# Kernel tuning notes

Hardware: AMD Instinct MI355X
Metric: run time of the kernel (lower is better)

The kernel has to match this reference:

```python
import jax, jax.numpy as jnp
import numpy as np

VOCAB, HID, EMB = 32000, 8, 32
SEQ, BATCH = 64, 64


def setup_inputs() -> dict:
    key = jax.random.key(0)
    ks = jax.random.split(key, 16)
    D = EMB + HID
    def lin(k, fan_in, fan_out):
        # mimic nn.Linear default init: U(-1/sqrt(fan_in), 1/sqrt(fan_in))
        lim = 1.0 / np.sqrt(fan_in)
        kw, kb = jax.random.split(k)
        W = jax.random.uniform(kw, (fan_in, fan_out), jnp.float32, -lim, lim)
        b = jax.random.uniform(kb, (fan_out,), jnp.float32, -lim, lim)
        return W, b
    x = jax.random.randint(ks[0], (SEQ, BATCH), 0, VOCAB)
    embeddings = jax.random.normal(ks[1], (VOCAB, EMB), jnp.float32)
    Wz1, bz1 = lin(ks[2], D, 1)
    Wr1, br1 = lin(ks[3], D, 1)
    Wh1, bh1 = lin(ks[4], D, HID)
    Wz2, bz2 = lin(ks[5], D, 1)
    Wr2, br2 = lin(ks[6], D, 1)
    Wh2, bh2 = lin(ks[7], D, HID)
    Wout, bout = lin(ks[8], 2 * HID, VOCAB)
    return dict(x=x, embeddings=embeddings,
                Wz1=Wz1, bz1=bz1, Wr1=Wr1, br1=br1, Wh1=Wh1, bh1=bh1,
                Wz2=Wz2, bz2=bz2, Wr2=Wr2, br2=br2, Wh2=Wh2, bh2=bh2,
                Wout=Wout, bout=bout)


def _gru_scan(enc, Wz, bz, Wr, br, Wh, bh):
    # enc: [T, B, E]; emits the PRE-update hidden state at each step, matching
    # the original (total_h[t] = h before the step-t update; last update unused).
    B = enc.shape[1]
    H = Wh.shape[1]
    h0 = jnp.zeros((B, H), enc.dtype)
    def step(h, e):
        cat = jnp.concatenate([h, e], axis=1)          # [B, H+E]
        z = jax.nn.sigmoid(cat @ Wz + bz)              # [B, 1] -> broadcast over H
        r = jax.nn.sigmoid(cat @ Wr + br)
        h_cand = jnp.tanh(jnp.concatenate([r * h, e], axis=1) @ Wh + bh)
        h_new = (1.0 - z) * h + z * h_cand
        return h_new, h
    _, hs = jax.lax.scan(step, h0, enc)
    return hs                                          # [T, B, H]


def reference(x, embeddings, Wz1, bz1, Wr1, br1, Wh1, bh1,
              Wz2, bz2, Wr2, br2, Wh2, bh2, Wout, bout):
    enc = embeddings[x]                                # [T, B, E]
    h1 = _gru_scan(enc, Wz1, bz1, Wr1, br1, Wh1, bh1)  # forward direction
    h2 = _gru_scan(enc[::-1], Wz2, bz2, Wr2, br2, Wh2, bh2)[::-1]  # backward
    total_h = jnp.concatenate([h1, h2], axis=2)        # [T, B, 2H]
    logits = total_h @ Wout + bout                     # [T, B, V]
    return jax.nn.log_softmax(logits, axis=2)
```

## Files before the change

kernel.cpp:

```cpp
#include <hip/hip_runtime.h>

#define T 64
#define B 64
#define V 32000
#define E 32
#define H 8
#define PSTR 12

typedef float f32x4 __attribute__((ext_vector_type(4)));

__device__ __forceinline__ float fast_rcp(float x) { return __builtin_amdgcn_rcpf(x); }
__device__ __forceinline__ float sigmoid_f(float x) { return fast_rcp(1.0f + __expf(-x)); }
__device__ __forceinline__ float tanh_f(float x) { return 1.0f - 2.0f * fast_rcp(__expf(2.0f * x) + 1.0f); }

__global__ void __launch_bounds__(64) precompute_kernel(
    const int* __restrict__ x, const float* __restrict__ emb,
    const float* __restrict__ Wz1, const float* __restrict__ bz1,
    const float* __restrict__ Wr1, const float* __restrict__ br1,
    const float* __restrict__ Wh1, const float* __restrict__ bh1,
    const float* __restrict__ Wz2, const float* __restrict__ bz2,
    const float* __restrict__ Wr2, const float* __restrict__ br2,
    const float* __restrict__ Wh2, const float* __restrict__ bh2,
    float* __restrict__ pre)
{
    const int i = blockIdx.x;
    const int dir = blockIdx.y;
    const int b = threadIdx.x;

    const float* Wz = dir ? Wz2 : Wz1;  const float* bz = dir ? bz2 : bz1;
    const float* Wr = dir ? Wr2 : Wr1;  const float* br = dir ? br2 : br1;
    const float* Wh = dir ? Wh2 : Wh1;  const float* bh = dir ? bh2 : bh1;

    const int pos = dir ? (T - 1 - i) : i;
    const int idx = x[pos * B + b];

    float e[E];
    const float4* e4p = reinterpret_cast<const float4*>(emb + (size_t)idx * E);
#pragma unroll
    for (int q = 0; q < E / 4; q++) {
        float4 t = e4p[q];
        e[q*4+0] = t.x; e[q*4+1] = t.y; e[q*4+2] = t.z; e[q*4+3] = t.w;
    }

    float az = bz[0], ar = br[0];
    float ah[H];
#pragma unroll
    for (int j = 0; j < H; j++) ah[j] = bh[j];

#pragma unroll
    for (int d = 0; d < E; d++) {
        const float ed = e[d];
        az += ed * Wz[H + d];
        ar += ed * Wr[H + d];
#pragma unroll
        for (int j = 0; j < H; j++) ah[j] += ed * Wh[(H + d) * H + j];
    }

    float* dst = pre + ((size_t)dir * T * B + i * B + b) * PSTR;
    float4 s0 = {az, ar, ah[0], ah[1]};
    float4 s1 = {ah[2], ah[3], ah[4], ah[5]};
    float4 s2 = {ah[6], ah[7], 0.0f, 0.0f};
    *reinterpret_cast<float4*>(dst + 0) = s0;
    *reinterpret_cast<float4*>(dst + 4) = s1;
    *reinterpret_cast<float4*>(dst + 8) = s2;
}

__global__ void __launch_bounds__(64) gru_scan_kernel(
    const float* __restrict__ Wz1, const float* __restrict__ Wr1, const float* __restrict__ Wh1,
    const float* __restrict__ Wz2, const float* __restrict__ Wr2, const float* __restrict__ Wh2,
    const float* __restrict__ pre, float* __restrict__ th)
{
    const int dir = blockIdx.x;
    const int b = threadIdx.x;
    const float* Wz = dir ? Wz2 : Wz1;
    const float* Wr = dir ? Wr2 : Wr1;
    const float* Wh = dir ? Wh2 : Wh1;

    float wzh[H], wrh[H], whh[H * H];
#pragma unroll
    for (int k = 0; k < H; k++) { wzh[k] = Wz[k]; wrh[k] = Wr[k]; }
#pragma unroll
    for (int d = 0; d < H; d++)
#pragma unroll
        for (int j = 0; j < H; j++) whh[d * H + j] = Wh[d * H + j];

    float h[H];
#pragma unroll
    for (int j = 0; j < H; j++) h[j] = 0.0f;

    const float* preD = pre + (size_t)dir * T * B * PSTR;
    const float4* p4 = reinterpret_cast<const float4*>(preD + (size_t)b * PSTR);
    float4 p0 = p4[0], p1 = p4[1], p2 = p4[2];

    for (int i = 0; i < T; i++) {
        const int pos = dir ? (T - 1 - i) : i;

        float* dst = th + ((size_t)pos * B + b) * 16 + dir * 8;
        float4 s0 = {h[0], h[1], h[2], h[3]};
        float4 s1 = {h[4], h[5], h[6], h[7]};
        *reinterpret_cast<float4*>(dst + 0) = s0;
        *reinterpret_cast<float4*>(dst + 4) = s1;

        const float az = p0.x, ar = p0.y;
        float ah[H] = {p0.z, p0.w, p1.x, p1.y, p1.z, p1.w, p2.x, p2.y};

        const int ni = (i < T - 1) ? (i + 1) : (T - 1);
        const float4* n4 = reinterpret_cast<const float4*>(preD + ((size_t)ni * B + b) * PSTR);
        p0 = n4[0]; p1 = n4[1]; p2 = n4[2];

        float zx = az, rx = ar;
#pragma unroll
        for (int k = 0; k < H; k++) { zx += h[k] * wzh[k]; rx += h[k] * wrh[k]; }
        const float z = sigmoid_f(zx);
        const float r = sigmoid_f(rx);

        float hc[H];
#pragma unroll
        for (int j = 0; j < H; j++) hc[j] = ah[j];
#pragma unroll
        for (int d = 0; d < H; d++) {
            const float rh = r * h[d];
#pragma unroll
            for (int j = 0; j < H; j++) hc[j] += rh * whh[d * H + j];
        }
#pragma unroll
        for (int j = 0; j < H; j++) {
            const float c = tanh_f(hc[j]);
            h[j] += z * (c - h[j]);
        }
    }
}

#define R 16
#define RS 8
#define NG (R / RS)
#define V4 (V / 4)
#define K3_THREADS 512
#define K3_WAVES (K3_THREADS / 64)

__device__ __forceinline__ float4 dot16(const float4 bb, const float4* w, const float* hrow) {
    float ax = bb.x, ay = bb.y, az = bb.z, aw = bb.w;
#pragma unroll
    for (int k4 = 0; k4 < 4; k4++) {
        const float4 hh = *reinterpret_cast<const float4*>(hrow + k4 * 4);
        ax += hh.x * w[k4*4+0].x; ay += hh.x * w[k4*4+0].y; az += hh.x * w[k4*4+0].z; aw += hh.x * w[k4*4+0].w;
        ax += hh.y * w[k4*4+1].x; ay += hh.y * w[k4*4+1].y; az += hh.y * w[k4*4+1].z; aw += hh.y * w[k4*4+1].w;
        ax += hh.z * w[k4*4+2].x; ay += hh.z * w[k4*4+2].y; az += hh.z * w[k4*4+2].z; aw += hh.z * w[k4*4+2].w;
        ax += hh.w * w[k4*4+3].x; ay += hh.w * w[k4*4+3].y; az += hh.w * w[k4*4+3].z; aw += hh.w * w[k4*4+3].w;
    }
    return {ax, ay, az, aw};
}

template<int SE0, int SEN, int ST0, int STN>
__device__ __forceinline__ void k3_phase(
    const float4* __restrict__ W4, const float4* __restrict__ b4p,
    float* __restrict__ out, const float (&hlds)[R][16],
    float (&l)[R], const float (&lse)[R], int tid, int row0)
{
    for (int v4 = tid; v4 < V4; v4 += K3_THREADS) {
        asm volatile("" ::: "memory");
        float4 w[16];
#pragma unroll
        for (int k = 0; k < 16; k++) w[k] = W4[(size_t)k * V4 + v4];
        const float4 bb = b4p[v4];

#pragma unroll
        for (int r = 0; r < STN; r++) {
            const int rr = ST0 + r;
            const float4 o = dot16(bb, w, &hlds[rr][0]);
            f32x4 res = {o.x - lse[rr], o.y - lse[rr], o.z - lse[rr], o.w - lse[rr]};
            f32x4* dst = reinterpret_cast<f32x4*>(out + ((size_t)(row0 + rr) * V4 + v4) * 4);
            __builtin_nontemporal_store(res, dst);
        }
#pragma unroll
        for (int r = 0; r < SEN; r++) {
            const int rr = SE0 + r;
            const float4 o = dot16(bb, w, &hlds[rr][0]);
            l[rr] += (__expf(o.x) + __expf(o.y)) + (__expf(o.z) + __expf(o.w));
        }
    }
}

template<int G0>
__device__ __forceinline__ void k3_reduce(
    float (&l)[R], float (&lse)[R],
    float (*red)[K3_WAVES][RS], int tid)
{
    float v[RS];
#pragma unroll
    for (int r = 0; r < RS; r++) {
        v[r] = l[G0 + r];
#pragma unroll
        for (int m = 1; m < 64; m <<= 1) v[r] += __shfl_xor(v[r], m, 64);
    }
    const int lane = tid & 63, wid = tid >> 6;
    if (lane == 0) {
#pragma unroll
        for (int r = 0; r < RS; r++) red[G0 / RS][wid][r] = v[r];
    }
    __syncthreads();
#pragma unroll
    for (int r = 0; r < RS; r++) {
        float t = 0.0f;
#pragma unroll
        for (int w = 0; w < K3_WAVES; w++) t += red[G0 / RS][w][r];
        lse[G0 + r] = logf(t);
    }
}

__global__ void __launch_bounds__(K3_THREADS) logits_kernel(
    const float* __restrict__ th, const float* __restrict__ Wout,
    const float* __restrict__ bout, float* __restrict__ out)
{
    __shared__ __align__(16) float hlds[R][16];
    __shared__ float red[NG][K3_WAVES][RS];

    const int tid = threadIdx.x;
    const int row0 = blockIdx.x * R;

    if (tid < R * 4) {
        reinterpret_cast<float4*>(hlds)[tid] =
            reinterpret_cast<const float4*>(th + (size_t)row0 * 16)[tid];
    }
    __syncthreads();

    const float4* W4 = reinterpret_cast<const float4*>(Wout);
    const float4* b4p = reinterpret_cast<const float4*>(bout);

    float l[R], lse[R];
#pragma unroll
    for (int r = 0; r < R; r++) { l[r] = 0.0f; lse[r] = 0.0f; }

    k3_phase<0,  RS, 0, 0 >(W4, b4p, out, hlds, l, lse, tid, row0);
    k3_reduce<0>(l, lse, red, tid);
    k3_phase<RS, RS, 0, RS>(W4, b4p, out, hlds, l, lse, tid, row0);
    k3_reduce<RS>(l, lse, red, tid);
    k3_phase<0, 0, RS, RS>(W4, b4p, out, hlds, l, lse, tid, row0);
}

extern "C" void kernel_launch(void* const* d_in, const int* in_sizes, int n_in,
                              void* d_out, int out_size, void* d_ws, size_t ws_size,
                              hipStream_t stream) {
    const int*   x    = (const int*)  d_in[0];
    const float* emb  = (const float*)d_in[1];
    const float* Wz1  = (const float*)d_in[2];  const float* bz1 = (const float*)d_in[3];
    const float* Wr1  = (const float*)d_in[4];  const float* br1 = (const float*)d_in[5];
    const float* Wh1  = (const float*)d_in[6];  const float* bh1 = (const float*)d_in[7];
    const float* Wz2  = (const float*)d_in[8];  const float* bz2 = (const float*)d_in[9];
    const float* Wr2  = (const float*)d_in[10]; const float* br2 = (const float*)d_in[11];
    const float* Wh2  = (const float*)d_in[12]; const float* bh2 = (const float*)d_in[13];
    const float* Wout = (const float*)d_in[14]; const float* bout = (const float*)d_in[15];
    float* out = (float*)d_out;

    float* ws = (float*)d_ws;
    float* th  = ws;
    float* pre = ws + (size_t)T * B * 16;

    precompute_kernel<<<dim3(T, 2), B, 0, stream>>>(
        x, emb, Wz1, bz1, Wr1, br1, Wh1, bh1, Wz2, bz2, Wr2, br2, Wh2, bh2, pre);
    gru_scan_kernel<<<2, B, 0, stream>>>(Wz1, Wr1, Wh1, Wz2, Wr2, Wh2, pre, th);
    logits_kernel<<<256, K3_THREADS, 0, stream>>>(th, Wout, bout, out);
}
```

Baseline: 705.7 us.

## Shrink logits row tile, keep hidden rows in registers, use regular stores

The logits kernel now processes 8 rows per block with 256 threads, giving 512 blocks, and holds each block's hidden vectors in registers rather than shared memory. It also drops the nontemporal stores and the compiler memory barrier. The GRU scan switches from fast-reciprocal sigmoid/tanh to the library expf and tanhf. Smaller tiles raise block count and occupancy, but each block now re-reads all of Wout for only 8 rows, which doubles weight traffic. The library math calls also slow the serial scan.

```diff
diff --git a/kernel.cpp b/kernel.cpp
--- a/kernel.cpp
+++ b/kernel.cpp
@@ -7,11 +7,7 @@
 #define H 8
 #define PSTR 12
 
-typedef float f32x4 __attribute__((ext_vector_type(4)));
-
 __device__ __forceinline__ float fast_rcp(float x) { return __builtin_amdgcn_rcpf(x); }
-__device__ __forceinline__ float sigmoid_f(float x) { return fast_rcp(1.0f + __expf(-x)); }
-__device__ __forceinline__ float tanh_f(float x) { return 1.0f - 2.0f * fast_rcp(__expf(2.0f * x) + 1.0f); }
 
 __global__ void __launch_bounds__(64) precompute_kernel(
     const int* __restrict__ x, const float* __restrict__ emb,
@@ -111,8 +107,8 @@
         float zx = az, rx = ar;
 #pragma unroll
         for (int k = 0; k < H; k++) { zx += h[k] * wzh[k]; rx += h[k] * wrh[k]; }
-        const float z = sigmoid_f(zx);
-        const float r = sigmoid_f(rx);
+        const float z = 1.0f / (1.0f + expf(-zx));
+        const float r = 1.0f / (1.0f + expf(-rx));
 
         float hc[H];
 #pragma unroll
@@ -125,24 +121,25 @@
         }
 #pragma unroll
         for (int j = 0; j < H; j++) {
-            const float c = tanh_f(hc[j]);
+            const float c = tanhf(hc[j]);
             h[j] += z * (c - h[j]);
         }
     }
 }
 
-#define R 16
-#define RS 8
-#define NG (R / RS)
+#define R 8
+#define RS 4
 #define V4 (V / 4)
-#define K3_THREADS 512
+#define K3_THREADS 256
 #define K3_WAVES (K3_THREADS / 64)
-
-__device__ __forceinline__ float4 dot16(const float4 bb, const float4* w, const float* hrow) {
+#define K3_BLOCKS ((T * B) / R)
+
+__device__ __forceinline__ float4 dot16r(const float4 bb, const float4* w,
+                                         const float4 (&hr)[4]) {
     float ax = bb.x, ay = bb.y, az = bb.z, aw = bb.w;
 #pragma unroll
     for (int k4 = 0; k4 < 4; k4++) {
-        const float4 hh = *reinterpret_cast<const float4*>(hrow + k4 * 4);
+        const float4 hh = hr[k4];
         ax += hh.x * w[k4*4+0].x; ay += hh.x * w[k4*4+0].y; az += hh.x * w[k4*4+0].z; aw += hh.x * w[k4*4+0].w;
         ax += hh.y * w[k4*4+1].x; ay += hh.y * w[k4*4+1].y; az += hh.y * w[k4*4+1].z; aw += hh.y * w[k4*4+1].w;
         ax += hh.z * w[k4*4+2].x; ay += hh.z * w[k4*4+2].y; az += hh.z * w[k4*4+2].z; aw += hh.z * w[k4*4+2].w;
@@ -154,11 +151,11 @@
 template<int SE0, int SEN, int ST0, int STN>
 __device__ __forceinline__ void k3_phase(
     const float4* __restrict__ W4, const float4* __restrict__ b4p,
-    float* __restrict__ out, const float (&hlds)[R][16],
+    float* __restrict__ out, const float4 (&h)[R][4],
     float (&l)[R], const float (&lse)[R], int tid, int row0)
 {
+    float4* out4 = reinterpret_cast<float4*>(out);
     for (int v4 = tid; v4 < V4; v4 += K3_THREADS) {
-        asm volatile("" ::: "memory");
         float4 w[16];
 #pragma unroll
         for (int k = 0; k < 16; k++) w[k] = W4[(size_t)k * V4 + v4];
@@ -167,15 +164,14 @@
 #pragma unroll
         for (int r = 0; r < STN; r++) {
             const int rr = ST0 + r;
-            const float4 o = dot16(bb, w, &hlds[rr][0]);
-            f32x4 res = {o.x - lse[rr], o.y - lse[rr], o.z - lse[rr], o.w - lse[rr]};
-            f32x4* dst = reinterpret_cast<f32x4*>(out + ((size_t)(row0 + rr) * V4 + v4) * 4);
-            __builtin_nontemporal_store(res, dst);
+            const float4 o = dot16r(bb, w, h[rr]);
+            float4 res = {o.x - lse[rr], o.y - lse[rr], o.z - lse[rr], o.w - lse[rr]};
+            out4[(size_t)(row0 + rr) * V4 + v4] = res;
         }
 #pragma unroll
         for (int r = 0; r < SEN; r++) {
             const int rr = SE0 + r;
-            const float4 o = dot16(bb, w, &hlds[rr][0]);
+            const float4 o = dot16r(bb, w, h[rr]);
             l[rr] += (__expf(o.x) + __expf(o.y)) + (__expf(o.z) + __expf(o.w));
         }
     }
@@ -208,21 +204,22 @@
     }
 }
 
-__global__ void __launch_bounds__(K3_THREADS) logits_kernel(
+__global__ void __launch_bounds__(K3_THREADS, 2) logits_kernel(
     const float* __restrict__ th, const float* __restrict__ Wout,
     const float* __restrict__ bout, float* __restrict__ out)
 {
-    __shared__ __align__(16) float hlds[R][16];
-    __shared__ float red[NG][K3_WAVES][RS];
+    __shared__ float red[R / RS][K3_WAVES][RS];
 
     const int tid = threadIdx.x;
     const int row0 = blockIdx.x * R;
 
-    if (tid < R * 4) {
-        reinterpret_cast<float4*>(hlds)[tid] =
-            reinterpret_cast<const float4*>(th + (size_t)row0 * 16)[tid];
-    }
-    __syncthreads();
+    float4 h[R][4];
+    const float4* th4 = reinterpret_cast<const float4*>(th);
+#pragma unroll
+    for (int r = 0; r < R; r++)
+#pragma unroll
+        for (int q = 0; q < 4; q++)
+            h[r][q] = th4[(size_t)(row0 + r) * 4 + q];
 
     const float4* W4 = reinterpret_cast<const float4*>(Wout);
     const float4* b4p = reinterpret_cast<const float4*>(bout);
@@ -231,11 +228,11 @@
 #pragma unroll
     for (int r = 0; r < R; r++) { l[r] = 0.0f; lse[r] = 0.0f; }
 
-    k3_phase<0,  RS, 0, 0 >(W4, b4p, out, hlds, l, lse, tid, row0);
+    k3_phase<0,  RS, 0, 0 >(W4, b4p, out, h, l, lse, tid, row0);
     k3_reduce<0>(l, lse, red, tid);
-    k3_phase<RS, RS, 0, RS>(W4, b4p, out, hlds, l, lse, tid, row0);
+    k3_phase<RS, RS, 0, RS>(W4, b4p, out, h, l, lse, tid, row0);
     k3_reduce<RS>(l, lse, red, tid);
-    k3_phase<0, 0, RS, RS>(W4, b4p, out, hlds, l, lse, tid, row0);
+    k3_phase<0, 0, RS, RS>(W4, b4p, out, h, l, lse, tid, row0);
 }
 
 extern "C" void kernel_launch(void* const* d_in, const int* in_sizes, int n_in,
@@ -259,5 +256,5 @@
     precompute_kernel<<<dim3(T, 2), B, 0, stream>>>(
         x, emb, Wz1, bz1, Wr1, br1, Wh1, bh1, Wz2, bz2, Wr2, br2, Wh2, bh2, pre);
     gru_scan_kernel<<<2, B, 0, stream>>>(Wz1, Wr1, Wh1, Wz2, Wr2, Wh2, pre, th);
-    logits_kernel<<<256, K3_THREADS, 0, stream>>>(th, Wout, bout, out);
-}
+    logits_kernel<<<K3_BLOCKS, K3_THREADS, 0, stream>>>(th, Wout, bout, out);
+}
```

After: 786.8 us. 11.5% more time.
